# Performance work log

Hardware: AMD Instinct MI355X
Metric: run time of the kernel (lower is better)

The kernel has to match this reference:

```python
import jax, jax.numpy as jnp
import numpy as np

B, N, D_IN, D_OUT = 16, 2048, 128, 128

def setup_inputs() -> dict:
    key = jax.random.key(0)
    ks = jax.random.split(key, 8)
    x = jax.random.normal(ks[0], (B, N, D_IN), dtype=jnp.float32)
    adj = jax.random.randint(ks[1], (N, N), 0, 2).astype(jnp.float32)
    # Conv1d(kernel_size=1) weights, PyTorch default uniform init scale
    s_emb = 1.0 / np.sqrt(D_IN)
    W_emb = jax.random.uniform(ks[2], (D_OUT, D_IN), jnp.float32, -s_emb, s_emb)
    b_emb = jax.random.uniform(ks[3], (D_OUT,), jnp.float32, -s_emb, s_emb)
    s_qk = 1.0 / np.sqrt(D_OUT)
    w_q = jax.random.uniform(ks[4], (D_OUT,), jnp.float32, -s_qk, s_qk)
    b_q = jax.random.uniform(ks[5], (1,), jnp.float32, -s_qk, s_qk)
    w_k = jax.random.uniform(ks[6], (D_OUT,), jnp.float32, -s_qk, s_qk)
    b_k = jax.random.uniform(ks[7], (1,), jnp.float32, -s_qk, s_qk)
    return {"x": x, "adj": adj, "W_emb": W_emb, "b_emb": b_emb,
            "w_q": w_q, "b_q": b_q, "w_k": w_k, "b_k": b_k}

def reference(x, adj, W_emb, b_emb, w_q, b_q, w_k, b_k):
    # emb_conv: 1x1 conv over node dim == per-node linear  [B,N,D_out]
    seq_fts = jnp.einsum('bni,oi->bno', x, W_emb) + b_emb
    # q_conv / k_conv: project to scalar per node  [B,N]
    q = jnp.einsum('bnd,d->bn', seq_fts, w_q) + b_q  # f_1_t squeezed
    k = jnp.einsum('bnd,d->bn', seq_fts, w_k) + b_k  # f_2_t squeezed
    # f[b,i,j] = f_1_t[b,0,j] + f_2_t^T[b,i,0] = q[b,j] + k[b,i]
    f = k[:, :, None] + q[:, None, :]                 # [B,N,N]
    f = jax.nn.leaky_relu(adj[None, :, :] * f, negative_slope=0.01)
    coefs = jax.nn.softmax(f, axis=1)                 # softmax over dim=1 (rows)
    vals = jnp.einsum('bij,bjd->bid', coefs, seq_fts)  # [B,N,D_out]
    return vals
```

## Files before the change

### kernel.cpp

```cpp
#include <hip/hip_runtime.h>
#include <hip/hip_bf16.h>
#include <stdint.h>

#define B_ 16
#define N_ 2048
#define D_ 128

typedef __bf16 bf16_t;
typedef bf16_t bf16x8 __attribute__((ext_vector_type(8)));
typedef float f32x4 __attribute__((ext_vector_type(4)));

__global__ __launch_bounds__(256) void k_pack_adj(const float* __restrict__ adj,
                                                  unsigned int* __restrict__ bits) {
    int t = blockIdx.x * 256 + threadIdx.x;
    float v = adj[t];
    unsigned long long m = __ballot(v > 0.5f);
    if ((t & 63) == 0) {
        int i = t >> 11;
        int j = t & 2047;
        bits[i * 64 + (j >> 5)]     = (unsigned int)m;
        bits[i * 64 + (j >> 5) + 1] = (unsigned int)(m >> 32);
    }
}

__global__ __launch_bounds__(256, 2) void k_emb(const float* __restrict__ x,
                                                const float* __restrict__ W,
                                                const float* __restrict__ be,
                                                const float* __restrict__ wq,
                                                const float* __restrict__ bq,
                                                const float* __restrict__ wk,
                                                const float* __restrict__ bk,
                                                bf16_t* __restrict__ Pb,
                                                float* __restrict__ qa, float* __restrict__ ka,
                                                float* __restrict__ Eq, float* __restrict__ eqs,
                                                float* __restrict__ Ek, float* __restrict__ eks) {
    __shared__ float xs[32][68];
    __shared__ float ws[32][132];
    __shared__ float qs[64], ks[64];
    int b  = blockIdx.y;
    int n0 = blockIdx.x * 64;
    int tid = threadIdx.x;
    int tx = tid & 15, ty = tid >> 4;
    if (tid < 64) { qs[tid] = 0.f; ks[tid] = 0.f; }

    float acc[4][8] = {};
    f32x4 xr[2], wr[4];

    auto loadregs = [&](int kc) {
#pragma unroll
        for (int s = 0; s < 2; ++s) {
            int p = tid + 256 * s;
            int n = p >> 3, kq = p & 7;
            xr[s] = *(const f32x4*)(x + ((size_t)(b * N_ + n0 + n)) * D_ + kc * 32 + kq * 4);
        }
#pragma unroll
        for (int s = 0; s < 4; ++s) {
            int p = tid + 256 * s;
            int d = p >> 3, kq = p & 7;
            wr[s] = *(const f32x4*)(W + (size_t)d * D_ + kc * 32 + kq * 4);
        }
    };
    auto writelds = [&]() {
#pragma unroll
        for (int s = 0; s < 2; ++s) {
            int p = tid + 256 * s;
            int n = p >> 3, kq = p & 7;
#pragma unroll
            for (int u = 0; u < 4; ++u) xs[kq * 4 + u][n] = xr[s][u];
        }
#pragma unroll
        for (int s = 0; s < 4; ++s) {
            int p = tid + 256 * s;
            int d = p >> 3, kq = p & 7;
#pragma unroll
            for (int u = 0; u < 4; ++u) ws[kq * 4 + u][d] = wr[s][u];
        }
    };

    loadregs(0);
    for (int kc = 0; kc < 4; ++kc) {
        writelds();
        __syncthreads();
        if (kc < 3) loadregs(kc + 1);
#pragma unroll 4
        for (int k = 0; k < 32; ++k) {
            f32x4 xv  = *(const f32x4*)&xs[k][tx * 4];
            f32x4 wv0 = *(const f32x4*)&ws[k][ty * 8];
            f32x4 wv1 = *(const f32x4*)&ws[k][ty * 8 + 4];
#pragma unroll
            for (int i = 0; i < 4; ++i)
#pragma unroll
                for (int j = 0; j < 8; ++j)
                    acc[i][j] += xv[i] * ((j < 4) ? wv0[j] : wv1[j - 4]);
        }
        __syncthreads();
    }

    float qp[4] = {}, kp[4] = {};
#pragma unroll
    for (int j = 0; j < 8; ++j) {
        int d = ty * 8 + j;
        float bj  = be[d];
        float wqj = wq[d];
        float wkj = wk[d];
        f32x4 o;
        bf16_t ob[4];
#pragma unroll
        for (int i = 0; i < 4; ++i) {
            o[i] = acc[i][j] + bj;
            qp[i] += o[i] * wqj;
            kp[i] += o[i] * wkj;
            ob[i] = (bf16_t)o[i];
        }
        *(uint2*)(Pb + ((size_t)b * D_ + d) * N_ + n0 + tx * 4) = *(uint2*)ob;
    }
#pragma unroll
    for (int i = 0; i < 4; ++i) {
        atomicAdd(&qs[tx * 4 + i], qp[i]);
        atomicAdd(&ks[tx * 4 + i], kp[i]);
    }
    __syncthreads();
    if (tid < 64) {
        int idx = b * N_ + n0 + tid;
        float aq = qs[tid] + bq[0];
        float ak = ks[tid] + bk[0];
        qa[idx] = aq;          ka[idx] = ak;
        Eq[idx] = expf(aq);    eqs[idx] = expf(0.01f * aq);
        Ek[idx] = expf(ak);    eks[idx] = expf(0.01f * ak);
    }
}

__global__ __launch_bounds__(256) void k_denom(const unsigned int* __restrict__ bits,
                                               const float* __restrict__ qa,
                                               const float* __restrict__ ka,
                                               const float* __restrict__ Eq,
                                               const float* __restrict__ eqs,
                                               const float* __restrict__ Ek,
                                               const float* __restrict__ eks,
                                               float* __restrict__ denom) {
    int jt  = blockIdx.x;
    int b   = blockIdx.y;
    int seg = blockIdx.z;
    int j = jt * 256 + threadIdx.x;
    float qj  = qa[b * N_ + j];
    float Eqj = Eq[b * N_ + j];
    float eqj = eqs[b * N_ + j];
    int shift = j & 31;
    int wid   = j >> 5;
    float acc = 0.f;
    int i0 = seg * 256;
#pragma unroll 16
    for (int i = i0; i < i0 + 256; ++i) {
        float kk  = ka[b * N_ + i];
        float Ekk = Ek[b * N_ + i];
        float ekk = eks[b * N_ + i];
        unsigned int w = bits[i * 64 + wid];
        float z  = kk + qj;
        float f1 = z > 0.f ? Ekk : ekk;
        float f2 = z > 0.f ? Eqj : eqj;
        float v  = f1 * f2;
        acc += ((w >> shift) & 1u) ? v : 1.0f;
    }
    atomicAdd(&denom[b * N_ + j], acc);
}

__global__ __launch_bounds__(256) void k_post(const float* __restrict__ denom,
                                              const float* __restrict__ Eq,
                                              const float* __restrict__ eqs,
                                              float* __restrict__ rd,
                                              float* __restrict__ Eqr,
                                              float* __restrict__ eqr) {
    int t = blockIdx.x * 256 + threadIdx.x;
    float r = 1.0f / denom[t];
    rd[t]  = r;
    Eqr[t] = Eq[t] * r;
    eqr[t] = eqs[t] * r;
}

__global__ __launch_bounds__(256, 2) void k_attn(const float* __restrict__ qa,
                                                 const float* __restrict__ ka,
                                                 const float* __restrict__ Ek,
                                                 const float* __restrict__ eks,
                                                 const float* __restrict__ rd,
                                                 const float* __restrict__ Eqr,
                                                 const float* __restrict__ eqr,
                                                 const unsigned int* __restrict__ bits,
                                                 const bf16_t* __restrict__ Pb,
                                                 float* __restrict__ out) {
    __shared__ __align__(16) bf16_t ldsB[2][128 * 64];
    __shared__ __align__(16) bf16_t ldsA[4 * 2 * 64 * 8];
    int b     = blockIdx.y;
    int ibase = blockIdx.x * 64;
    int tid   = threadIdx.x;
    int w     = tid >> 6;
    int lane  = tid & 63;
    int m16   = lane & 15;
    int quad  = lane >> 4;
    int ig    = w & 1;
    int dg    = w >> 1;

    int iA = ibase + (2 * ig) * 16 + m16;
    int iB = iA + 16;
    float mkR0 = -ka[b * N_ + iA], mkR1 = -ka[b * N_ + iB];
    float EkR0 = Ek[b * N_ + iA],  EkR1 = Ek[b * N_ + iB];
    float ekR0 = eks[b * N_ + iA], ekR1 = eks[b * N_ + iB];
    const unsigned int* brA = bits + (size_t)iA * 64;
    const unsigned int* brB = bits + (size_t)iB * 64;
    const float* qp  = qa  + b * N_;
    const float* Erp = Eqr + b * N_;
    const float* erp = eqr + b * N_;
    const float* rdp = rd  + b * N_;
    const bf16_t* PtB = Pb + (size_t)b * D_ * N_;

    f32x4 acc[2][4];
#pragma unroll
    for (int c = 0; c < 2; ++c)
#pragma unroll
        for (int nt = 0; nt < 4; ++nt) acc[c][nt] = (f32x4){0.f, 0.f, 0.f, 0.f};

    f32x4 qv4[2][2], Er4[2][2], er4[2][2], rd4[2][2];
    unsigned int mA[2], mB[2];

    auto ldj = [&](int par, int jb) {
        int j0 = jb + dg * 32 + quad * 8;
        qv4[par][0] = *(const f32x4*)(qp  + j0);
        qv4[par][1] = *(const f32x4*)(qp  + j0 + 4);
        Er4[par][0] = *(const f32x4*)(Erp + j0);
        Er4[par][1] = *(const f32x4*)(Erp + j0 + 4);
        er4[par][0] = *(const f32x4*)(erp + j0);
        er4[par][1] = *(const f32x4*)(erp + j0 + 4);
        rd4[par][0] = *(const f32x4*)(rdp + j0);
        rd4[par][1] = *(const f32x4*)(rdp + j0 + 4);
        mA[par] = brA[(jb >> 5) + dg];
        mB[par] = brB[(jb >> 5) + dg];
    };

    auto stage = [&](int bufi, int jb) {
#pragma unroll
        for (int t = 0; t < 4; ++t) {
            int off = t * 4096 + tid * 16;
            int d   = off >> 7;
            int g   = ((off & 127) >> 4) ^ (d & 7);
            const bf16_t* gp = PtB + (size_t)d * N_ + jb + g * 8;
            __builtin_amdgcn_global_load_lds(
                (const __attribute__((address_space(1))) void*)gp,
                (__attribute__((address_space(3))) void*)((char*)(&ldsB[bufi][0]) + off),
                16, 0, 0);
        }
    };

    stage(0, 0);
    ldj(0, 0);
    __syncthreads();
    int buf = 0;
#pragma unroll 1
    for (int s2 = 0; s2 < N_ / 128; ++s2) {
#pragma unroll
        for (int par = 0; par < 2; ++par) {
            int step = s2 * 2 + par;
            int jb = step * 64;
            if (step + 1 < N_ / 64) {
                ldj(par ^ 1, jb + 64);
                stage(buf ^ 1, jb + 64);
            }

            bf16x8 afA, afB;
#pragma unroll
            for (int t = 0; t < 8; ++t) {
                float qv = (t < 4) ? qv4[par][0][t] : qv4[par][1][t - 4];
                float Er = (t < 4) ? Er4[par][0][t] : Er4[par][1][t - 4];
                float er = (t < 4) ? er4[par][0][t] : er4[par][1][t - 4];
                float rj = (t < 4) ? rd4[par][0][t] : rd4[par][1][t - 4];
                int bit = quad * 8 + t;
                {
                    bool c = qv > mkR0;
                    float v = (c ? EkR0 : ekR0) * (c ? Er : er);
                    afA[t] = (bf16_t)(((mA[par] >> bit) & 1u) ? v : rj);
                }
                {
                    bool c = qv > mkR1;
                    float v = (c ? EkR1 : ekR1) * (c ? Er : er);
                    afB[t] = (bf16_t)(((mB[par] >> bit) & 1u) ? v : rj);
                }
            }
            *(bf16x8*)((char*)ldsA + ((((2 * ig + 0) * 2 + dg) * 64 + lane) * 16)) = afA;
            *(bf16x8*)((char*)ldsA + ((((2 * ig + 1) * 2 + dg) * 64 + lane) * 16)) = afB;

            asm volatile("s_waitcnt lgkmcnt(0)\n\ts_barrier" ::: "memory");

            {
                int cph = ((dg * 4 + quad) ^ (m16 & 7)) * 8;
#pragma unroll
                for (int nt = 0; nt < 4; ++nt) {
                    int d = dg * 64 + nt * 16 + m16;
                    bf16x8 bf = *(const bf16x8*)&ldsB[buf][d * 64 + cph];
                    acc[0][nt] = __builtin_amdgcn_mfma_f32_16x16x32_bf16(afA, bf, acc[0][nt], 0, 0, 0);
                    acc[1][nt] = __builtin_amdgcn_mfma_f32_16x16x32_bf16(afB, bf, acc[1][nt], 0, 0, 0);
                }
            }
            {
                int oh = 1 - dg;
                bf16x8 a0 = *(const bf16x8*)((char*)ldsA + ((((2 * ig + 0) * 2 + oh) * 64 + lane) * 16));
                bf16x8 a1 = *(const bf16x8*)((char*)ldsA + ((((2 * ig + 1) * 2 + oh) * 64 + lane) * 16));
                int cph = ((oh * 4 + quad) ^ (m16 & 7)) * 8;
#pragma unroll
                for (int nt = 0; nt < 4; ++nt) {
                    int d = dg * 64 + nt * 16 + m16;
                    bf16x8 bf = *(const bf16x8*)&ldsB[buf][d * 64 + cph];
                    acc[0][nt] = __builtin_amdgcn_mfma_f32_16x16x32_bf16(a0, bf, acc[0][nt], 0, 0, 0);
                    acc[1][nt] = __builtin_amdgcn_mfma_f32_16x16x32_bf16(a1, bf, acc[1][nt], 0, 0, 0);
                }
            }
            __syncthreads();
            buf ^= 1;
        }
    }

#pragma unroll
    for (int c = 0; c < 2; ++c) {
        int irow = ibase + (2 * ig + c) * 16 + quad * 4;
#pragma unroll
        for (int nt = 0; nt < 4; ++nt) {
            int d = dg * 64 + nt * 16 + m16;
#pragma unroll
            for (int r = 0; r < 4; ++r)
                out[((size_t)b * N_ + irow + r) * D_ + d] = acc[c][nt][r];
        }
    }
}

extern "C" void kernel_launch(void* const* d_in, const int* in_sizes, int n_in,
                              void* d_out, int out_size, void* d_ws, size_t ws_size,
                              hipStream_t stream) {
    const float* x   = (const float*)d_in[0];
    const float* adj = (const float*)d_in[1];
    const float* W   = (const float*)d_in[2];
    const float* be  = (const float*)d_in[3];
    const float* wq  = (const float*)d_in[4];
    const float* bq  = (const float*)d_in[5];
    const float* wk  = (const float*)d_in[6];
    const float* bk  = (const float*)d_in[7];
    float* out = (float*)d_out;

    char* ws = (char*)d_ws;
    size_t off = 0;
    bf16_t* Pb = (bf16_t*)(ws + off); off += (size_t)B_ * D_ * N_ * 2;
    float* qa  = (float*)(ws + off);  off += (size_t)B_ * N_ * 4;
    float* ka  = (float*)(ws + off);  off += (size_t)B_ * N_ * 4;
    float* denom = (float*)(ws + off); off += (size_t)B_ * N_ * 4;
    float* Eq  = (float*)(ws + off);  off += (size_t)B_ * N_ * 4;
    float* eqs = (float*)(ws + off);  off += (size_t)B_ * N_ * 4;
    float* Ek  = (float*)(ws + off);  off += (size_t)B_ * N_ * 4;
    float* eks = (float*)(ws + off);  off += (size_t)B_ * N_ * 4;
    float* rd  = (float*)(ws + off);  off += (size_t)B_ * N_ * 4;
    float* Eqr = (float*)(ws + off);  off += (size_t)B_ * N_ * 4;
    float* eqr = (float*)(ws + off);  off += (size_t)B_ * N_ * 4;
    unsigned int* bits = (unsigned int*)(ws + off); off += (size_t)N_ * 64 * 4;

    hipMemsetAsync(denom, 0, (size_t)B_ * N_ * 4, stream);

    k_pack_adj<<<N_ * N_ / 256, 256, 0, stream>>>(adj, bits);
    k_emb<<<dim3(N_ / 64, B_), 256, 0, stream>>>(x, W, be, wq, bq, wk, bk,
                                                 Pb, qa, ka, Eq, eqs, Ek, eks);
    k_denom<<<dim3(8, 16, 8), 256, 0, stream>>>(bits, qa, ka, Eq, eqs, Ek, eks, denom);
    k_post<<<B_ * N_ / 256, 256, 0, stream>>>(denom, Eq, eqs, rd, Eqr, eqr);
    k_attn<<<dim3(N_ / 64, B_), 256, 0, stream>>>(qa, ka, Ek, eks, rd, Eqr, eqr,
                                                  bits, Pb, out);
}
```

Measured before the change: 187.8 us.

## Halve attention row tile to 32 rows, raise occupancy, fold denom zeroing into emb

```diff
diff --git a/kernel.cpp b/kernel.cpp
--- a/kernel.cpp
+++ b/kernel.cpp
@@ -33,7 +33,8 @@
                                                 bf16_t* __restrict__ Pb,
                                                 float* __restrict__ qa, float* __restrict__ ka,
                                                 float* __restrict__ Eq, float* __restrict__ eqs,
-                                                float* __restrict__ Ek, float* __restrict__ eks) {
+                                                float* __restrict__ Ek, float* __restrict__ eks,
+                                                float* __restrict__ denom) {
     __shared__ float xs[32][68];
     __shared__ float ws[32][132];
     __shared__ float qs[64], ks[64];
@@ -127,6 +128,7 @@
         qa[idx] = aq;          ka[idx] = ak;
         Eq[idx] = expf(aq);    eqs[idx] = expf(0.01f * aq);
         Ek[idx] = expf(ak);    eks[idx] = expf(0.01f * ak);
+        denom[idx] = 0.f;
     }
 }
 
@@ -177,7 +179,7 @@
     eqr[t] = eqs[t] * r;
 }
 
-__global__ __launch_bounds__(256, 2) void k_attn(const float* __restrict__ qa,
+__global__ __launch_bounds__(256, 4) void k_attn(const float* __restrict__ qa,
                                                  const float* __restrict__ ka,
                                                  const float* __restrict__ Ek,
                                                  const float* __restrict__ eks,
@@ -188,41 +190,39 @@
                                                  const bf16_t* __restrict__ Pb,
                                                  float* __restrict__ out) {
     __shared__ __align__(16) bf16_t ldsB[2][128 * 64];
-    __shared__ __align__(16) bf16_t ldsA[4 * 2 * 64 * 8];
+    __shared__ __align__(16) bf16_t ldsA[2 * 2 * 64 * 8];
     int b     = blockIdx.y;
-    int ibase = blockIdx.x * 64;
+    int ibase = blockIdx.x * 32;
     int tid   = threadIdx.x;
     int w     = tid >> 6;
     int lane  = tid & 63;
     int m16   = lane & 15;
     int quad  = lane >> 4;
-    int ig    = w & 1;
-    int dg    = w >> 1;
-
-    int iA = ibase + (2 * ig) * 16 + m16;
-    int iB = iA + 16;
-    float mkR0 = -ka[b * N_ + iA], mkR1 = -ka[b * N_ + iB];
-    float EkR0 = Ek[b * N_ + iA],  EkR1 = Ek[b * N_ + iB];
-    float ekR0 = eks[b * N_ + iA], ekR1 = eks[b * N_ + iB];
+    int cA    = w & 1;
+    int hA    = w >> 1;
+
+    int iA = ibase + cA * 16 + m16;
+    float mkR = -ka[b * N_ + iA];
+    float EkR = Ek[b * N_ + iA];
+    float ekR = eks[b * N_ + iA];
     const unsigned int* brA = bits + (size_t)iA * 64;
-    const unsigned int* brB = bits + (size_t)iB * 64;
     const float* qp  = qa  + b * N_;
     const float* Erp = Eqr + b * N_;
     const float* erp = eqr + b * N_;
     const float* rdp = rd  + b * N_;
     const bf16_t* PtB = Pb + (size_t)b * D_ * N_;
 
-    f32x4 acc[2][4];
+    f32x4 acc[2][2];
 #pragma unroll
     for (int c = 0; c < 2; ++c)
 #pragma unroll
-        for (int nt = 0; nt < 4; ++nt) acc[c][nt] = (f32x4){0.f, 0.f, 0.f, 0.f};
+        for (int nt = 0; nt < 2; ++nt) acc[c][nt] = (f32x4){0.f, 0.f, 0.f, 0.f};
 
     f32x4 qv4[2][2], Er4[2][2], er4[2][2], rd4[2][2];
-    unsigned int mA[2], mB[2];
+    unsigned int mA[2];
 
     auto ldj = [&](int par, int jb) {
-        int j0 = jb + dg * 32 + quad * 8;
+        int j0 = jb + hA * 32 + quad * 8;
         qv4[par][0] = *(const f32x4*)(qp  + j0);
         qv4[par][1] = *(const f32x4*)(qp  + j0 + 4);
         Er4[par][0] = *(const f32x4*)(Erp + j0);
@@ -231,8 +231,7 @@
         er4[par][1] = *(const f32x4*)(erp + j0 + 4);
         rd4[par][0] = *(const f32x4*)(rdp + j0);
         rd4[par][1] = *(const f32x4*)(rdp + j0 + 4);
-        mA[par] = brA[(jb >> 5) + dg];
-        mB[par] = brB[(jb >> 5) + dg];
+        mA[par] = brA[(jb >> 5) + hA];
     };
 
     auto stage = [&](int bufi, int jb) {
@@ -264,7 +263,7 @@
                 stage(buf ^ 1, jb + 64);
             }
 
-            bf16x8 afA, afB;
+            bf16x8 afA;
 #pragma unroll
             for (int t = 0; t < 8; ++t) {
                 float qv = (t < 4) ? qv4[par][0][t] : qv4[par][1][t - 4];
@@ -272,43 +271,29 @@
                 float er = (t < 4) ? er4[par][0][t] : er4[par][1][t - 4];
                 float rj = (t < 4) ? rd4[par][0][t] : rd4[par][1][t - 4];
                 int bit = quad * 8 + t;
-                {
-                    bool c = qv > mkR0;
-                    float v = (c ? EkR0 : ekR0) * (c ? Er : er);
-                    afA[t] = (bf16_t)(((mA[par] >> bit) & 1u) ? v : rj);
-                }
-                {
-                    bool c = qv > mkR1;
-                    float v = (c ? EkR1 : ekR1) * (c ? Er : er);
-                    afB[t] = (bf16_t)(((mB[par] >> bit) & 1u) ? v : rj);
-                }
+                bool c = qv > mkR;
+                float v = (c ? EkR : ekR) * (c ? Er : er);
+                afA[t] = (bf16_t)(((mA[par] >> bit) & 1u) ? v : rj);
             }
-            *(bf16x8*)((char*)ldsA + ((((2 * ig + 0) * 2 + dg) * 64 + lane) * 16)) = afA;
-            *(bf16x8*)((char*)ldsA + ((((2 * ig + 1) * 2 + dg) * 64 + lane) * 16)) = afB;
+            *(bf16x8*)((char*)ldsA + (((cA * 2 + hA) * 64 + lane) * 16)) = afA;
 
             asm volatile("s_waitcnt lgkmcnt(0)\n\ts_barrier" ::: "memory");
 
-            {
-                int cph = ((dg * 4 + quad) ^ (m16 & 7)) * 8;
-#pragma unroll
-                for (int nt = 0; nt < 4; ++nt) {
-                    int d = dg * 64 + nt * 16 + m16;
+            bf16x8 af[2][2];
+#pragma unroll
+            for (int c = 0; c < 2; ++c)
+#pragma unroll
+                for (int h = 0; h < 2; ++h)
+                    af[c][h] = *(const bf16x8*)((char*)ldsA + (((c * 2 + h) * 64 + lane) * 16));
+#pragma unroll
+            for (int h = 0; h < 2; ++h) {
+                int cph = ((h * 4 + quad) ^ (m16 & 7)) * 8;
+#pragma unroll
+                for (int nt = 0; nt < 2; ++nt) {
+                    int d = w * 32 + nt * 16 + m16;
                     bf16x8 bf = *(const bf16x8*)&ldsB[buf][d * 64 + cph];
-                    acc[0][nt] = __builtin_amdgcn_mfma_f32_16x16x32_bf16(afA, bf, acc[0][nt], 0, 0, 0);
-                    acc[1][nt] = __builtin_amdgcn_mfma_f32_16x16x32_bf16(afB, bf, acc[1][nt], 0, 0, 0);
-                }
-            }
-            {
-                int oh = 1 - dg;
-                bf16x8 a0 = *(const bf16x8*)((char*)ldsA + ((((2 * ig + 0) * 2 + oh) * 64 + lane) * 16));
-                bf16x8 a1 = *(const bf16x8*)((char*)ldsA + ((((2 * ig + 1) * 2 + oh) * 64 + lane) * 16));
-                int cph = ((oh * 4 + quad) ^ (m16 & 7)) * 8;
-#pragma unroll
-                for (int nt = 0; nt < 4; ++nt) {
-                    int d = dg * 64 + nt * 16 + m16;
-                    bf16x8 bf = *(const bf16x8*)&ldsB[buf][d * 64 + cph];
-                    acc[0][nt] = __builtin_amdgcn_mfma_f32_16x16x32_bf16(a0, bf, acc[0][nt], 0, 0, 0);
-                    acc[1][nt] = __builtin_amdgcn_mfma_f32_16x16x32_bf16(a1, bf, acc[1][nt], 0, 0, 0);
+                    acc[0][nt] = __builtin_amdgcn_mfma_f32_16x16x32_bf16(af[0][h], bf, acc[0][nt], 0, 0, 0);
+                    acc[1][nt] = __builtin_amdgcn_mfma_f32_16x16x32_bf16(af[1][h], bf, acc[1][nt], 0, 0, 0);
                 }
             }
             __syncthreads();
@@ -318,10 +303,10 @@
 
 #pragma unroll
     for (int c = 0; c < 2; ++c) {
-        int irow = ibase + (2 * ig + c) * 16 + quad * 4;
-#pragma unroll
-        for (int nt = 0; nt < 4; ++nt) {
-            int d = dg * 64 + nt * 16 + m16;
+        int irow = ibase + c * 16 + quad * 4;
+#pragma unroll
+        for (int nt = 0; nt < 2; ++nt) {
+            int d = w * 32 + nt * 16 + m16;
 #pragma unroll
             for (int r = 0; r < 4; ++r)
                 out[((size_t)b * N_ + irow + r) * D_ + d] = acc[c][nt][r];
@@ -357,13 +342,11 @@
     float* eqr = (float*)(ws + off);  off += (size_t)B_ * N_ * 4;
     unsigned int* bits = (unsigned int*)(ws + off); off += (size_t)N_ * 64 * 4;
 
-    hipMemsetAsync(denom, 0, (size_t)B_ * N_ * 4, stream);
-
     k_pack_adj<<<N_ * N_ / 256, 256, 0, stream>>>(adj, bits);
     k_emb<<<dim3(N_ / 64, B_), 256, 0, stream>>>(x, W, be, wq, bq, wk, bk,
-                                                 Pb, qa, ka, Eq, eqs, Ek, eks);
+                                                 Pb, qa, ka, Eq, eqs, Ek, eks, denom);
     k_denom<<<dim3(8, 16, 8), 256, 0, stream>>>(bits, qa, ka, Eq, eqs, Ek, eks, denom);
     k_post<<<B_ * N_ / 256, 256, 0, stream>>>(denom, Eq, eqs, rd, Eqr, eqr);
-    k_attn<<<dim3(N_ / 64, B_), 256, 0, stream>>>(qa, ka, Ek, eks, rd, Eqr, eqr,
+    k_attn<<<dim3(N_ / 32, B_), 256, 0, stream>>>(qa, ka, Ek, eks, rd, Eqr, eqr,
                                                   bits, Pb, out);
 }
```

After: 255.6 us. +36.1%, slower.

## Peel attention pipeline tail, relax waitcnts for prefetch overlap, fold denom memset

Applied to the files above, without the earlier changes.

```diff
diff --git a/kernel.cpp b/kernel.cpp
--- a/kernel.cpp
+++ b/kernel.cpp
@@ -33,7 +33,8 @@
                                                 bf16_t* __restrict__ Pb,
                                                 float* __restrict__ qa, float* __restrict__ ka,
                                                 float* __restrict__ Eq, float* __restrict__ eqs,
-                                                float* __restrict__ Ek, float* __restrict__ eks) {
+                                                float* __restrict__ Ek, float* __restrict__ eks,
+                                                float* __restrict__ denom) {
     __shared__ float xs[32][68];
     __shared__ float ws[32][132];
     __shared__ float qs[64], ks[64];
@@ -127,6 +128,7 @@
         qa[idx] = aq;          ka[idx] = ak;
         Eq[idx] = expf(aq);    eqs[idx] = expf(0.01f * aq);
         Ek[idx] = expf(ak);    eks[idx] = expf(0.01f * ak);
+        denom[idx] = 0.f;
     }
 }
 
@@ -249,71 +251,96 @@
         }
     };
 
+    auto agen = [&](int par, bf16x8& afA, bf16x8& afB) {
+#pragma unroll
+        for (int t = 0; t < 8; ++t) {
+            float qv = (t < 4) ? qv4[par][0][t] : qv4[par][1][t - 4];
+            float Er = (t < 4) ? Er4[par][0][t] : Er4[par][1][t - 4];
+            float er = (t < 4) ? er4[par][0][t] : er4[par][1][t - 4];
+            float rj = (t < 4) ? rd4[par][0][t] : rd4[par][1][t - 4];
+            int bit = quad * 8 + t;
+            {
+                bool c = qv > mkR0;
+                float v = (c ? EkR0 : ekR0) * (c ? Er : er);
+                afA[t] = (bf16_t)(((mA[par] >> bit) & 1u) ? v : rj);
+            }
+            {
+                bool c = qv > mkR1;
+                float v = (c ? EkR1 : ekR1) * (c ? Er : er);
+                afB[t] = (bf16_t)(((mB[par] >> bit) & 1u) ? v : rj);
+            }
+        }
+        *(bf16x8*)((char*)ldsA + ((((2 * ig + 0) * 2 + dg) * 64 + lane) * 16)) = afA;
+        *(bf16x8*)((char*)ldsA + ((((2 * ig + 1) * 2 + dg) * 64 + lane) * 16)) = afB;
+    };
+
+    auto mfma_phase = [&](int buf, const bf16x8& afA, const bf16x8& afB) {
+        {
+            int cph = ((dg * 4 + quad) ^ (m16 & 7)) * 8;
+#pragma unroll
+            for (int nt = 0; nt < 4; ++nt) {
+                int d = dg * 64 + nt * 16 + m16;
+                bf16x8 bf = *(const bf16x8*)&ldsB[buf][d * 64 + cph];
+                acc[0][nt] = __builtin_amdgcn_mfma_f32_16x16x32_bf16(afA, bf, acc[0][nt], 0, 0, 0);
+                acc[1][nt] = __builtin_amdgcn_mfma_f32_16x16x32_bf16(afB, bf, acc[1][nt], 0, 0, 0);
+            }
+        }
+        {
+            int oh = 1 - dg;
+            bf16x8 a0 = *(const bf16x8*)((char*)ldsA + ((((2 * ig + 0) * 2 + oh) * 64 + lane) * 16));
+            bf16x8 a1 = *(const bf16x8*)((char*)ldsA + ((((2 * ig + 1) * 2 + oh) * 64 + lane) * 16));
+            int cph = ((oh * 4 + quad) ^ (m16 & 7)) * 8;
+#pragma unroll
+            for (int nt = 0; nt < 4; ++nt) {
+                int d = dg * 64 + nt * 16 + m16;
+                bf16x8 bf = *(const bf16x8*)&ldsB[buf][d * 64 + cph];
+                acc[0][nt] = __builtin_amdgcn_mfma_f32_16x16x32_bf16(a0, bf, acc[0][nt], 0, 0, 0);
+                acc[1][nt] = __builtin_amdgcn_mfma_f32_16x16x32_bf16(a1, bf, acc[1][nt], 0, 0, 0);
+            }
+        }
+    };
+
     stage(0, 0);
     ldj(0, 0);
-    __syncthreads();
     int buf = 0;
 #pragma unroll 1
-    for (int s2 = 0; s2 < N_ / 128; ++s2) {
+    for (int s2 = 0; s2 < 15; ++s2) {
 #pragma unroll
         for (int par = 0; par < 2; ++par) {
-            int step = s2 * 2 + par;
-            int jb = step * 64;
-            if (step + 1 < N_ / 64) {
-                ldj(par ^ 1, jb + 64);
-                stage(buf ^ 1, jb + 64);
-            }
+            int jb = (s2 * 2 + par) * 64;
+            ldj(par ^ 1, jb + 64);
+            stage(buf ^ 1, jb + 64);
 
             bf16x8 afA, afB;
-#pragma unroll
-            for (int t = 0; t < 8; ++t) {
-                float qv = (t < 4) ? qv4[par][0][t] : qv4[par][1][t - 4];
-                float Er = (t < 4) ? Er4[par][0][t] : Er4[par][1][t - 4];
-                float er = (t < 4) ? er4[par][0][t] : er4[par][1][t - 4];
-                float rj = (t < 4) ? rd4[par][0][t] : rd4[par][1][t - 4];
-                int bit = quad * 8 + t;
-                {
-                    bool c = qv > mkR0;
-                    float v = (c ? EkR0 : ekR0) * (c ? Er : er);
-                    afA[t] = (bf16_t)(((mA[par] >> bit) & 1u) ? v : rj);
-                }
-                {
-                    bool c = qv > mkR1;
-                    float v = (c ? EkR1 : ekR1) * (c ? Er : er);
-                    afB[t] = (bf16_t)(((mB[par] >> bit) & 1u) ? v : rj);
-                }
-            }
-            *(bf16x8*)((char*)ldsA + ((((2 * ig + 0) * 2 + dg) * 64 + lane) * 16)) = afA;
-            *(bf16x8*)((char*)ldsA + ((((2 * ig + 1) * 2 + dg) * 64 + lane) * 16)) = afB;
-
-            asm volatile("s_waitcnt lgkmcnt(0)\n\ts_barrier" ::: "memory");
-
-            {
-                int cph = ((dg * 4 + quad) ^ (m16 & 7)) * 8;
-#pragma unroll
-                for (int nt = 0; nt < 4; ++nt) {
-                    int d = dg * 64 + nt * 16 + m16;
-                    bf16x8 bf = *(const bf16x8*)&ldsB[buf][d * 64 + cph];
-                    acc[0][nt] = __builtin_amdgcn_mfma_f32_16x16x32_bf16(afA, bf, acc[0][nt], 0, 0, 0);
-                    acc[1][nt] = __builtin_amdgcn_mfma_f32_16x16x32_bf16(afB, bf, acc[1][nt], 0, 0, 0);
-                }
-            }
-            {
-                int oh = 1 - dg;
-                bf16x8 a0 = *(const bf16x8*)((char*)ldsA + ((((2 * ig + 0) * 2 + oh) * 64 + lane) * 16));
-                bf16x8 a1 = *(const bf16x8*)((char*)ldsA + ((((2 * ig + 1) * 2 + oh) * 64 + lane) * 16));
-                int cph = ((oh * 4 + quad) ^ (m16 & 7)) * 8;
-#pragma unroll
-                for (int nt = 0; nt < 4; ++nt) {
-                    int d = dg * 64 + nt * 16 + m16;
-                    bf16x8 bf = *(const bf16x8*)&ldsB[buf][d * 64 + cph];
-                    acc[0][nt] = __builtin_amdgcn_mfma_f32_16x16x32_bf16(a0, bf, acc[0][nt], 0, 0, 0);
-                    acc[1][nt] = __builtin_amdgcn_mfma_f32_16x16x32_bf16(a1, bf, acc[1][nt], 0, 0, 0);
-                }
-            }
-            __syncthreads();
+            agen(par, afA, afB);
+            asm volatile("s_waitcnt vmcnt(14) lgkmcnt(0)" ::: "memory");
+            __builtin_amdgcn_s_barrier();
+
+            mfma_phase(buf, afA, afB);
+
+            asm volatile("s_waitcnt lgkmcnt(0)" ::: "memory");
+            __builtin_amdgcn_s_barrier();
             buf ^= 1;
         }
+    }
+    {
+        ldj(1, 31 * 64);
+        stage(buf ^ 1, 31 * 64);
+        bf16x8 afA, afB;
+        agen(0, afA, afB);
+        asm volatile("s_waitcnt vmcnt(14) lgkmcnt(0)" ::: "memory");
+        __builtin_amdgcn_s_barrier();
+        mfma_phase(buf, afA, afB);
+        asm volatile("s_waitcnt lgkmcnt(0)" ::: "memory");
+        __builtin_amdgcn_s_barrier();
+        buf ^= 1;
+    }
+    {
+        bf16x8 afA, afB;
+        agen(1, afA, afB);
+        asm volatile("s_waitcnt vmcnt(0) lgkmcnt(0)" ::: "memory");
+        __builtin_amdgcn_s_barrier();
+        mfma_phase(buf, afA, afB);
     }
 
 #pragma unroll
@@ -357,11 +384,9 @@
     float* eqr = (float*)(ws + off);  off += (size_t)B_ * N_ * 4;
     unsigned int* bits = (unsigned int*)(ws + off); off += (size_t)N_ * 64 * 4;
 
-    hipMemsetAsync(denom, 0, (size_t)B_ * N_ * 4, stream);
-
     k_pack_adj<<<N_ * N_ / 256, 256, 0, stream>>>(adj, bits);
     k_emb<<<dim3(N_ / 64, B_), 256, 0, stream>>>(x, W, be, wq, bq, wk, bk,
-                                                 Pb, qa, ka, Eq, eqs, Ek, eks);
+                                                 Pb, qa, ka, Eq, eqs, Ek, eks, denom);
     k_denom<<<dim3(8, 16, 8), 256, 0, stream>>>(bits, qa, ka, Eq, eqs, Ek, eks, denom);
     k_post<<<B_ * N_ / 256, 256, 0, stream>>>(denom, Eq, eqs, rd, Eqr, eqr);
     k_attn<<<dim3(N_ / 64, B_), 256, 0, stream>>>(qa, ka, Ek, eks, rd, Eqr, eqr,
```

After: 186.3 us. No clear change (-0.8%).
